# Optimization experiments

Hardware: AMD Instinct MI355X
Metric: run time of the kernel (lower is better)

The kernel has to match this reference:

```python
import jax, jax.numpy as jnp
import numpy as np

B = 512     # graphs
NPG = 128   # nodes per graph
EPG = 2048  # edges per graph (avg degree 16)
IN = 128
HID = 128
K = 64      # ceil(0.5 * 128), SAGPooling ratio=0.5


def setup_inputs() -> dict:
    key = jax.random.key(0)
    ks = jax.random.split(key, 8)
    n_total = B * NPG
    x = jax.random.normal(ks[0], (n_total, IN), dtype=jnp.float32)
    # intra-graph random edges (PyG batching: edges never cross graphs)
    g = jnp.repeat(jnp.arange(B, dtype=jnp.int32), EPG)
    src = g * NPG + jax.random.randint(ks[1], (B * EPG,), 0, NPG, dtype=jnp.int32)
    dst = g * NPG + jax.random.randint(ks[2], (B * EPG,), 0, NPG, dtype=jnp.int32)
    edge_index = jnp.stack([src, dst], axis=0)
    batch = jnp.repeat(jnp.arange(B, dtype=jnp.int32), NPG)
    # params (glorot-ish scaling)
    W1 = jax.random.normal(ks[3], (IN, HID), dtype=jnp.float32) / np.sqrt(IN)
    b1 = jnp.zeros((HID,), dtype=jnp.float32)
    Ws = jax.random.normal(ks[4], (HID, 1), dtype=jnp.float32) / np.sqrt(HID)
    bs = jnp.zeros((1,), dtype=jnp.float32)
    Wlin = jax.random.normal(ks[5], (HID, HID), dtype=jnp.float32) / np.sqrt(HID)
    blin = jnp.zeros((HID,), dtype=jnp.float32)
    return {"x": x, "edge_index": edge_index, "batch": batch,
            "W1": W1, "b1": b1, "Ws": Ws, "bs": bs, "Wlin": Wlin, "blin": blin}


def _gcn_conv(x, src, dst, W, b, n):
    # PyG GCNConv: add self loops, symmetric deg^-1/2 norm, aggregate src->dst
    h = x @ W  # [n, out]
    loop = jnp.arange(n, dtype=src.dtype)
    s = jnp.concatenate([src, loop])
    d = jnp.concatenate([dst, loop])
    deg = jax.ops.segment_sum(jnp.ones(d.shape[0], dtype=x.dtype), d, num_segments=n)
    norm = jax.lax.rsqrt(deg)[s] * jax.lax.rsqrt(deg)[d]  # deg >= 1 via self loops
    msg = h[s] * norm[:, None]
    return jax.ops.segment_sum(msg, d, num_segments=n) + b


def reference(x, edge_index, batch, W1, b1, Ws, bs, Wlin, blin):
    n = x.shape[0]
    src, dst = edge_index[0], edge_index[1]
    # conv1 + relu
    h = jax.nn.relu(_gcn_conv(x, src, dst, W1, b1, n))  # [n, HID]
    # SAGPooling: score via GCNConv(HID -> 1)
    score = _gcn_conv(h, src, dst, Ws, bs, n)[:, 0]  # [n]
    # per-graph top-k on raw score (graphs are uniform NPG nodes -> dense top_k)
    score2 = score.reshape(B, NPG)
    top_v, top_i = jax.lax.top_k(score2, K)  # [B, K]
    h3 = h.reshape(B, NPG, HID)
    h_kept = jnp.take_along_axis(h3, top_i[:, :, None], axis=1)  # [B, K, HID]
    h_kept = h_kept * jnp.tanh(top_v)[:, :, None]  # x[perm] * tanh(score[perm])
    # global_mean_pool over kept nodes of each graph
    pooled = h_kept.mean(axis=1)  # [B, HID]
    return pooled @ Wlin + blin
```

## Files before the change

kernel.cpp:

```cpp
#include <hip/hip_runtime.h>
#include <math.h>

#define NPG  128
#define HID  128
#define KSEL 64
#define NT   256
#define HS   132
#define AS   17
#define FS   516

typedef __attribute__((ext_vector_type(8))) __bf16 bfrag;
typedef __attribute__((ext_vector_type(4))) float f4;

static __device__ __forceinline__ unsigned short bf2us(__bf16 b) {
    union { unsigned short s; __bf16 b; } x; x.b = b; return x.s;
}

__global__ __launch_bounds__(NT, 2) void sagpool_fused(
    const float* __restrict__ x,
    const int*   __restrict__ esrc,
    const int*   __restrict__ edst,
    const float* __restrict__ W1,
    const float* __restrict__ b1,
    const float* __restrict__ Ws,
    const float* __restrict__ bsp,
    const float* __restrict__ Wlin,
    const float* __restrict__ blin,
    float* __restrict__ out,
    int epg)
{
    __shared__ __align__(16) unsigned HpT[HID * HS];
    __shared__ __align__(16) unsigned AdjN[NPG * AS];
    __shared__ __align__(16) float rsl[NPG];
    __shared__ __align__(16) float spl[NPG];
    __shared__ __align__(16) float scl[NPG];
    __shared__ __align__(16) float wgt[NPG];
    __shared__ __align__(16) float pp[4 * HID];

    const int g = blockIdx.x, t = threadIdx.x;
    const int node0 = g * NPG;
    const long e0 = (long)g * epg;
    const int lane = t & 63, wv = t >> 6;
    const int n16 = lane & 15, quad = lane >> 4;
    const int m0 = wv * 32;

    int es[8], ed[8];
#pragma unroll
    for (int i = 0; i < 8; ++i) {
        int e = i * NT + t;
        es[i] = esrc[e0 + e] - node0;
        ed[i] = edst[e0 + e] - node0;
    }
    bfrag ah[8], al[8];
    {
        const float* xw = x + (long)(node0 + m0) * HID;
#pragma unroll
        for (int rt = 0; rt < 2; ++rt)
#pragma unroll
            for (int ks = 0; ks < 4; ++ks) {
                const float* xr = xw + (rt * 16 + n16) * HID + ks * 32 + quad * 8;
                float4 a = *reinterpret_cast<const float4*>(xr);
                float4 b = *reinterpret_cast<const float4*>(xr + 4);
                float vv[8] = {a.x, a.y, a.z, a.w, b.x, b.y, b.z, b.w};
                const int r = rt * 4 + ks;
#pragma unroll
                for (int j = 0; j < 8; ++j) {
                    __bf16 hb = (__bf16)vv[j];
                    ah[r][j] = hb;
                    al[r][j] = (__bf16)(vv[j] - (float)hb);
                }
            }
    }
    float b1v[8], wsv[8];
#pragma unroll
    for (int ct = 0; ct < 8; ++ct) {
        b1v[ct] = b1[ct * 16 + n16];
        wsv[ct] = Ws[ct * 16 + n16];
    }
    const float bsv = bsp[0];

    for (int i = t; i < NPG * AS; i += NT) AdjN[i] = 0u;
    __syncthreads();

    {
#pragma unroll
        for (int i = 0; i < 4; ++i) {
            const int tau = i * NT + t;
            const int ng = tau & 31, kg = tau >> 5;
            const int n0 = ng * 4, k0 = kg * 4;
            f4 r[4];
#pragma unroll
            for (int e = 0; e < 4; ++e)
                r[e] = *reinterpret_cast<const f4*>(W1 + (k0 + e) * HID + n0);
            const int p   = (k0 >> 5) * 8 + (n0 >> 4);
            const int j0h = (k0 & 7) >> 1;
            const int l0  = ((k0 >> 3) & 3) * 16;
#pragma unroll
            for (int c = 0; c < 4; ++c) {
                const int lane0 = l0 + (n0 & 15) + c;
                unsigned hs[4], ls[4];
#pragma unroll
                for (int e = 0; e < 4; ++e) {
                    float v = r[e][c];
                    __bf16 hb = (__bf16)v;
                    __bf16 lb = (__bf16)(v - (float)hb);
                    hs[e] = bf2us(hb); ls[e] = bf2us(lb);
                }
                uint2 sh, sl;
                sh.x = hs[0] | (hs[1] << 16); sh.y = hs[2] | (hs[3] << 16);
                sl.x = ls[0] | (ls[1] << 16); sl.y = ls[2] | (ls[3] << 16);
                const int base = p * FS + lane0 * 4 + j0h;
                *reinterpret_cast<uint2*>(&HpT[base])       = sh;
                *reinterpret_cast<uint2*>(&HpT[base + 256]) = sl;
            }
        }
    }
#pragma unroll
    for (int i = 0; i < 8; ++i)
        atomicAdd(&AdjN[ed[i] * AS + (es[i] >> 3)], 1u << ((es[i] & 7) * 4));
    __syncthreads();

    if (t < NPG) {
        unsigned* row = &AdjN[t * AS];
        unsigned sum = 0;
#pragma unroll
        for (int w = 0; w < 16; ++w) {
            unsigned u = row[w];
            unsigned b = (u & 0x0F0F0F0Fu) + ((u >> 4) & 0x0F0F0F0Fu);
            sum += (b * 0x01010101u) >> 24;
        }
        rsl[t] = rsqrtf((float)(sum + 1));
        row[t >> 3] += 1u << ((t & 7) * 4);
    }

    f4 acc[2][8];
#pragma unroll
    for (int rt = 0; rt < 2; ++rt)
#pragma unroll
        for (int ct = 0; ct < 8; ++ct) {
            acc[rt][ct].x = 0.f; acc[rt][ct].y = 0.f;
            acc[rt][ct].z = 0.f; acc[rt][ct].w = 0.f;
        }
#pragma unroll
    for (int ks = 0; ks < 4; ++ks)
#pragma unroll
        for (int ct = 0; ct < 8; ++ct) {
            const unsigned* fp = &HpT[(ks * 8 + ct) * FS + lane * 4];
            bfrag bh = *reinterpret_cast<const bfrag*>(fp);
            bfrag bl = *reinterpret_cast<const bfrag*>(fp + 256);
#pragma unroll
            for (int rt = 0; rt < 2; ++rt) {
                const int r = rt * 4 + ks;
                acc[rt][ct] = __builtin_amdgcn_mfma_f32_16x16x32_bf16(ah[r], bh, acc[rt][ct], 0, 0, 0);
                acc[rt][ct] = __builtin_amdgcn_mfma_f32_16x16x32_bf16(al[r], bh, acc[rt][ct], 0, 0, 0);
                acc[rt][ct] = __builtin_amdgcn_mfma_f32_16x16x32_bf16(ah[r], bl, acc[rt][ct], 0, 0, 0);
            }
        }
    __syncthreads();

#pragma unroll
    for (int rt = 0; rt < 2; ++rt) {
        const int mb = m0 + rt * 16 + quad * 4;
        f4 rs4 = *reinterpret_cast<const f4*>(&rsl[mb]);
#pragma unroll
        for (int ct = 0; ct < 8; ++ct) {
            unsigned hs[4], ls[4];
#pragma unroll
            for (int reg = 0; reg < 4; ++reg) {
                float v = acc[rt][ct][reg] * rs4[reg];
                __bf16 hb = (__bf16)v;
                __bf16 lb = (__bf16)(v - (float)hb);
                hs[reg] = bf2us(hb); ls[reg] = bf2us(lb);
            }
            uint2 sh, sl;
            sh.x = hs[0] | (hs[1] << 16); sh.y = hs[2] | (hs[3] << 16);
            sl.x = ls[0] | (ls[1] << 16); sl.y = ls[2] | (ls[3] << 16);
            const int rb = (ct * 16 + n16) * HS + (mb >> 1);
            *reinterpret_cast<uint2*>(&HpT[rb])      = sh;
            *reinterpret_cast<uint2*>(&HpT[rb + 64]) = sl;
        }
    }
    __syncthreads();

    f4 hacc[2][8];
#pragma unroll
    for (int mt = 0; mt < 2; ++mt)
#pragma unroll
        for (int ct = 0; ct < 8; ++ct) {
            hacc[mt][ct].x = 0.f; hacc[mt][ct].y = 0.f;
            hacc[mt][ct].z = 0.f; hacc[mt][ct].w = 0.f;
        }
#pragma unroll
    for (int ks = 0; ks < 4; ++ks) {
        bfrag af[2];
#pragma unroll
        for (int mt = 0; mt < 2; ++mt) {
            unsigned w = AdjN[(m0 + mt * 16 + n16) * AS + ks * 4 + quad];
#pragma unroll
            for (int j = 0; j < 8; ++j)
                af[mt][j] = (__bf16)(float)((w >> (4 * j)) & 15u);
        }
#pragma unroll
        for (int ct = 0; ct < 8; ++ct) {
            const unsigned* bp = &HpT[(ct * 16 + n16) * HS + ks * 16 + quad * 4];
            bfrag bh = *reinterpret_cast<const bfrag*>(bp);
            bfrag bl = *reinterpret_cast<const bfrag*>(bp + 64);
#pragma unroll
            for (int mt = 0; mt < 2; ++mt) {
                hacc[mt][ct] = __builtin_amdgcn_mfma_f32_16x16x32_bf16(af[mt], bh, hacc[mt][ct], 0, 0, 0);
                hacc[mt][ct] = __builtin_amdgcn_mfma_f32_16x16x32_bf16(af[mt], bl, hacc[mt][ct], 0, 0, 0);
            }
        }
    }

    f4 rsm[2];
#pragma unroll
    for (int mt = 0; mt < 2; ++mt)
        rsm[mt] = *reinterpret_cast<const f4*>(&rsl[m0 + mt * 16 + quad * 4]);
#pragma unroll
    for (int mt = 0; mt < 2; ++mt)
#pragma unroll
        for (int ct = 0; ct < 8; ++ct)
#pragma unroll
            for (int reg = 0; reg < 4; ++reg)
                hacc[mt][ct][reg] = fmaxf(hacc[mt][ct][reg] * rsm[mt][reg] + b1v[ct], 0.f);

    {
        float dot[2][4];
#pragma unroll
        for (int mt = 0; mt < 2; ++mt)
#pragma unroll
            for (int reg = 0; reg < 4; ++reg) dot[mt][reg] = 0.f;
#pragma unroll
        for (int ct = 0; ct < 8; ++ct)
#pragma unroll
            for (int mt = 0; mt < 2; ++mt)
#pragma unroll
                for (int reg = 0; reg < 4; ++reg)
                    dot[mt][reg] += hacc[mt][ct][reg] * wsv[ct];
#pragma unroll
        for (int d = 1; d < 16; d <<= 1)
#pragma unroll
            for (int mt = 0; mt < 2; ++mt)
#pragma unroll
                for (int reg = 0; reg < 4; ++reg)
                    dot[mt][reg] += __shfl_xor(dot[mt][reg], d, 64);
        if (n16 == 0) {
#pragma unroll
            for (int mt = 0; mt < 2; ++mt)
#pragma unroll
                for (int reg = 0; reg < 4; ++reg)
                    spl[m0 + mt * 16 + quad * 4 + reg] = rsm[mt][reg] * dot[mt][reg];
        }
    }
    __syncthreads();

    if (t < NPG) {
        const unsigned* row = &AdjN[t * AS];
        float sc = 0.f;
#pragma unroll
        for (int w = 0; w < 16; ++w) {
            unsigned u = row[w];
            const float* sp = &spl[w * 8];
            sc += (float)(u & 15u)         * sp[0] + (float)((u >> 4)  & 15u) * sp[1]
                + (float)((u >> 8)  & 15u) * sp[2] + (float)((u >> 12) & 15u) * sp[3]
                + (float)((u >> 16) & 15u) * sp[4] + (float)((u >> 20) & 15u) * sp[5]
                + (float)((u >> 24) & 15u) * sp[6] + (float)(u >> 28)         * sp[7];
        }
        scl[t] = rsl[t] * sc + bsv;
    } else {
        const int tt = t - NPG;
        const f4* WL4 = reinterpret_cast<const f4*>(Wlin);
        for (int ib = 0; ib < 4; ++ib) {
            f4 w[8];
#pragma unroll
            for (int u = 0; u < 8; ++u)
                w[u] = WL4[(ib * 8 + u) * 128 + tt];
#pragma unroll
            for (int u = 0; u < 8; ++u)
                *reinterpret_cast<f4*>(&HpT[((ib * 8 + u) * 128 + tt) * 4]) = w[u];
        }
    }
    __syncthreads();

    if (t < NPG) {
        float v = scl[t];
        int rank = 0;
#pragma unroll
        for (int j4 = 0; j4 < 32; ++j4) {
            float4 u = *reinterpret_cast<const float4*>(&scl[j4 * 4]);
            const int jb = j4 * 4;
            rank += (u.x > v || (u.x == v && jb     < t)) ? 1 : 0;
            rank += (u.y > v || (u.y == v && jb + 1 < t)) ? 1 : 0;
            rank += (u.z > v || (u.z == v && jb + 2 < t)) ? 1 : 0;
            rank += (u.w > v || (u.w == v && jb + 3 < t)) ? 1 : 0;
        }
        wgt[t] = (rank < KSEL) ? tanhf(v) * (1.0f / KSEL) : 0.f;
    }
    __syncthreads();

    {
        float p[8];
        f4 wm[2];
#pragma unroll
        for (int mt = 0; mt < 2; ++mt)
            wm[mt] = *reinterpret_cast<const f4*>(&wgt[m0 + mt * 16 + quad * 4]);
#pragma unroll
        for (int ct = 0; ct < 8; ++ct) {
            float s = 0.f;
#pragma unroll
            for (int mt = 0; mt < 2; ++mt)
#pragma unroll
                for (int reg = 0; reg < 4; ++reg)
                    s += wm[mt][reg] * hacc[mt][ct][reg];
            p[ct] = s;
        }
#pragma unroll
        for (int d = 16; d < 64; d <<= 1)
#pragma unroll
            for (int ct = 0; ct < 8; ++ct)
                p[ct] += __shfl_xor(p[ct], d, 64);
        if (quad == 0) {
#pragma unroll
            for (int ct = 0; ct < 8; ++ct)
                pp[wv * HID + ct * 16 + n16] = p[ct];
        }
    }
    __syncthreads();
    if (t < NPG)
        scl[t] = pp[t] + pp[HID + t] + pp[2 * HID + t] + pp[3 * HID + t];
    __syncthreads();

    {
        const int c4 = (t & 31) * 4, rg = t >> 5;
        f4 s4; s4.x = 0.f; s4.y = 0.f; s4.z = 0.f; s4.w = 0.f;
#pragma unroll 8
        for (int kk = 0; kk < 16; ++kk) {
            const int k = rg * 16 + kk;
            const f4 w = *reinterpret_cast<const f4*>(&HpT[k * HID + c4]);
            const float sk = scl[k];
            s4.x += sk * w.x; s4.y += sk * w.y;
            s4.z += sk * w.z; s4.w += sk * w.w;
        }
        float* part = reinterpret_cast<float*>(AdjN);
        *reinterpret_cast<f4*>(&part[rg * HID + c4]) = s4;
    }
    __syncthreads();
    if (t < NPG) {
        const float* part = reinterpret_cast<const float*>(AdjN);
        float s = blin[t];
#pragma unroll
        for (int r = 0; r < 8; ++r) s += part[r * HID + t];
        out[(long)g * HID + t] = s;
    }
}

extern "C" void kernel_launch(void* const* d_in, const int* in_sizes, int n_in,
                              void* d_out, int out_size, void* d_ws, size_t ws_size,
                              hipStream_t stream) {
    const float* x    = (const float*)d_in[0];
    const int*   ei   = (const int*)  d_in[1];
    const float* W1   = (const float*)d_in[3];
    const float* b1   = (const float*)d_in[4];
    const float* Ws   = (const float*)d_in[5];
    const float* bs   = (const float*)d_in[6];
    const float* Wlin = (const float*)d_in[7];
    const float* blin = (const float*)d_in[8];
    float* out = (float*)d_out;

    const int E = in_sizes[1] / 2;
    const int nnodes = in_sizes[0] / HID;
    const int B = nnodes / NPG;
    const int epg = E / B;

    sagpool_fused<<<B, NT, 0, stream>>>(x, ei, ei + E, W1, b1, Ws, bs,
                                        Wlin, blin, out, epg);
}
```

Measured before the change: 108.3 us.

## Double block size and split output column tiles across two wave groups

Raises the block to 512 threads (8 waves) and has each pair of waves split the 128 output columns in half. Both dense MFMA stages (x@W1 and the adjacency aggregation) and the pooling reduction now use half the column tiles per wave, with score partials summed from two shared-memory slices. Edge loading, W1 staging and the final Wlin product are redistributed across the extra threads. The aim is more waves per CU to hide latency, at the cost of each column half reloading the same x rows and a tighter register budget under launch_bounds(512,4), which may cause spills.

Measured after the change: 113.6 us. +4.9%, slower.

```diff
diff --git a/kernel.cpp b/kernel.cpp
--- a/kernel.cpp
+++ b/kernel.cpp
@@ -4,7 +4,7 @@
 #define NPG  128
 #define HID  128
 #define KSEL 64
-#define NT   256
+#define NT   512
 #define HS   132
 #define AS   17
 #define FS   516
@@ -16,7 +16,7 @@
     union { unsigned short s; __bf16 b; } x; x.b = b; return x.s;
 }
 
-__global__ __launch_bounds__(NT, 2) void sagpool_fused(
+__global__ __launch_bounds__(NT, 4) void sagpool_fused(
     const float* __restrict__ x,
     const int*   __restrict__ esrc,
     const int*   __restrict__ edst,
@@ -32,7 +32,7 @@
     __shared__ __align__(16) unsigned HpT[HID * HS];
     __shared__ __align__(16) unsigned AdjN[NPG * AS];
     __shared__ __align__(16) float rsl[NPG];
-    __shared__ __align__(16) float spl[NPG];
+    __shared__ __align__(16) float spl[2 * NPG];
     __shared__ __align__(16) float scl[NPG];
     __shared__ __align__(16) float wgt[NPG];
     __shared__ __align__(16) float pp[4 * HID];
@@ -41,12 +41,13 @@
     const int node0 = g * NPG;
     const long e0 = (long)g * epg;
     const int lane = t & 63, wv = t >> 6;
+    const int rt4 = wv & 3, ch = wv >> 2;
     const int n16 = lane & 15, quad = lane >> 4;
-    const int m0 = wv * 32;
-
-    int es[8], ed[8];
-#pragma unroll
-    for (int i = 0; i < 8; ++i) {
+    const int m0 = rt4 * 32;
+
+    int es[4], ed[4];
+#pragma unroll
+    for (int i = 0; i < 4; ++i) {
         int e = i * NT + t;
         es[i] = esrc[e0 + e] - node0;
         ed[i] = edst[e0 + e] - node0;
@@ -71,20 +72,13 @@
                 }
             }
     }
-    float b1v[8], wsv[8];
-#pragma unroll
-    for (int ct = 0; ct < 8; ++ct) {
-        b1v[ct] = b1[ct * 16 + n16];
-        wsv[ct] = Ws[ct * 16 + n16];
-    }
-    const float bsv = bsp[0];
 
     for (int i = t; i < NPG * AS; i += NT) AdjN[i] = 0u;
     __syncthreads();
 
     {
 #pragma unroll
-        for (int i = 0; i < 4; ++i) {
+        for (int i = 0; i < 2; ++i) {
             const int tau = i * NT + t;
             const int ng = tau & 31, kg = tau >> 5;
             const int n0 = ng * 4, k0 = kg * 4;
@@ -116,7 +110,7 @@
         }
     }
 #pragma unroll
-    for (int i = 0; i < 8; ++i)
+    for (int i = 0; i < 4; ++i)
         atomicAdd(&AdjN[ed[i] * AS + (es[i] >> 3)], 1u << ((es[i] & 7) * 4));
     __syncthreads();
 
@@ -133,27 +127,28 @@
         row[t >> 3] += 1u << ((t & 7) * 4);
     }
 
-    f4 acc[2][8];
+    f4 acc[2][4];
 #pragma unroll
     for (int rt = 0; rt < 2; ++rt)
 #pragma unroll
-        for (int ct = 0; ct < 8; ++ct) {
-            acc[rt][ct].x = 0.f; acc[rt][ct].y = 0.f;
-            acc[rt][ct].z = 0.f; acc[rt][ct].w = 0.f;
+        for (int c = 0; c < 4; ++c) {
+            acc[rt][c].x = 0.f; acc[rt][c].y = 0.f;
+            acc[rt][c].z = 0.f; acc[rt][c].w = 0.f;
         }
 #pragma unroll
     for (int ks = 0; ks < 4; ++ks)
 #pragma unroll
-        for (int ct = 0; ct < 8; ++ct) {
-            const unsigned* fp = &HpT[(ks * 8 + ct) * FS + lane * 4];
+        for (int c = 0; c < 4; ++c) {
+            const int ctg = ch * 4 + c;
+            const unsigned* fp = &HpT[(ks * 8 + ctg) * FS + lane * 4];
             bfrag bh = *reinterpret_cast<const bfrag*>(fp);
             bfrag bl = *reinterpret_cast<const bfrag*>(fp + 256);
 #pragma unroll
             for (int rt = 0; rt < 2; ++rt) {
                 const int r = rt * 4 + ks;
-                acc[rt][ct] = __builtin_amdgcn_mfma_f32_16x16x32_bf16(ah[r], bh, acc[rt][ct], 0, 0, 0);
-                acc[rt][ct] = __builtin_amdgcn_mfma_f32_16x16x32_bf16(al[r], bh, acc[rt][ct], 0, 0, 0);
-                acc[rt][ct] = __builtin_amdgcn_mfma_f32_16x16x32_bf16(ah[r], bl, acc[rt][ct], 0, 0, 0);
+                acc[rt][c] = __builtin_amdgcn_mfma_f32_16x16x32_bf16(ah[r], bh, acc[rt][c], 0, 0, 0);
+                acc[rt][c] = __builtin_amdgcn_mfma_f32_16x16x32_bf16(al[r], bh, acc[rt][c], 0, 0, 0);
+                acc[rt][c] = __builtin_amdgcn_mfma_f32_16x16x32_bf16(ah[r], bl, acc[rt][c], 0, 0, 0);
             }
         }
     __syncthreads();
@@ -163,11 +158,12 @@
         const int mb = m0 + rt * 16 + quad * 4;
         f4 rs4 = *reinterpret_cast<const f4*>(&rsl[mb]);
 #pragma unroll
-        for (int ct = 0; ct < 8; ++ct) {
+        for (int c = 0; c < 4; ++c) {
+            const int ctg = ch * 4 + c;
             unsigned hs[4], ls[4];
 #pragma unroll
             for (int reg = 0; reg < 4; ++reg) {
-                float v = acc[rt][ct][reg] * rs4[reg];
+                float v = acc[rt][c][reg] * rs4[reg];
                 __bf16 hb = (__bf16)v;
                 __bf16 lb = (__bf16)(v - (float)hb);
                 hs[reg] = bf2us(hb); ls[reg] = bf2us(lb);
@@ -175,110 +171,121 @@
             uint2 sh, sl;
             sh.x = hs[0] | (hs[1] << 16); sh.y = hs[2] | (hs[3] << 16);
             sl.x = ls[0] | (ls[1] << 16); sl.y = ls[2] | (ls[3] << 16);
-            const int rb = (ct * 16 + n16) * HS + (mb >> 1);
+            const int rb = (ctg * 16 + n16) * HS + (mb >> 1);
             *reinterpret_cast<uint2*>(&HpT[rb])      = sh;
             *reinterpret_cast<uint2*>(&HpT[rb + 64]) = sl;
         }
     }
     __syncthreads();
 
-    f4 hacc[2][8];
-#pragma unroll
-    for (int mt = 0; mt < 2; ++mt)
-#pragma unroll
-        for (int ct = 0; ct < 8; ++ct) {
-            hacc[mt][ct].x = 0.f; hacc[mt][ct].y = 0.f;
-            hacc[mt][ct].z = 0.f; hacc[mt][ct].w = 0.f;
+    float b1v[4], wsv[4];
+#pragma unroll
+    for (int c = 0; c < 4; ++c) {
+        b1v[c] = b1[(ch * 4 + c) * 16 + n16];
+        wsv[c] = Ws[(ch * 4 + c) * 16 + n16];
+    }
+    const float bsv = bsp[0];
+
+    f4 hacc[2][4];
+#pragma unroll
+    for (int rt = 0; rt < 2; ++rt)
+#pragma unroll
+        for (int c = 0; c < 4; ++c) {
+            hacc[rt][c].x = 0.f; hacc[rt][c].y = 0.f;
+            hacc[rt][c].z = 0.f; hacc[rt][c].w = 0.f;
         }
 #pragma unroll
     for (int ks = 0; ks < 4; ++ks) {
         bfrag af[2];
 #pragma unroll
-        for (int mt = 0; mt < 2; ++mt) {
-            unsigned w = AdjN[(m0 + mt * 16 + n16) * AS + ks * 4 + quad];
+        for (int rt = 0; rt < 2; ++rt) {
+            unsigned w = AdjN[(m0 + rt * 16 + n16) * AS + ks * 4 + quad];
 #pragma unroll
             for (int j = 0; j < 8; ++j)
-                af[mt][j] = (__bf16)(float)((w >> (4 * j)) & 15u);
-        }
-#pragma unroll
-        for (int ct = 0; ct < 8; ++ct) {
-            const unsigned* bp = &HpT[(ct * 16 + n16) * HS + ks * 16 + quad * 4];
+                af[rt][j] = (__bf16)(float)((w >> (4 * j)) & 15u);
+        }
+#pragma unroll
+        for (int c = 0; c < 4; ++c) {
+            const int ctg = ch * 4 + c;
+            const unsigned* bp = &HpT[(ctg * 16 + n16) * HS + ks * 16 + quad * 4];
             bfrag bh = *reinterpret_cast<const bfrag*>(bp);
             bfrag bl = *reinterpret_cast<const bfrag*>(bp + 64);
 #pragma unroll
-            for (int mt = 0; mt < 2; ++mt) {
-                hacc[mt][ct] = __builtin_amdgcn_mfma_f32_16x16x32_bf16(af[mt], bh, hacc[mt][ct], 0, 0, 0);
-                hacc[mt][ct] = __builtin_amdgcn_mfma_f32_16x16x32_bf16(af[mt], bl, hacc[mt][ct], 0, 0, 0);
+            for (int rt = 0; rt < 2; ++rt) {
+                hacc[rt][c] = __builtin_amdgcn_mfma_f32_16x16x32_bf16(af[rt], bh, hacc[rt][c], 0, 0, 0);
+                hacc[rt][c] = __builtin_amdgcn_mfma_f32_16x16x32_bf16(af[rt], bl, hacc[rt][c], 0, 0, 0);
             }
         }
     }
 
     f4 rsm[2];
 #pragma unroll
-    for (int mt = 0; mt < 2; ++mt)
-        rsm[mt] = *reinterpret_cast<const f4*>(&rsl[m0 + mt * 16 + quad * 4]);
-#pragma unroll
-    for (int mt = 0; mt < 2; ++mt)
-#pragma unroll
-        for (int ct = 0; ct < 8; ++ct)
+    for (int rt = 0; rt < 2; ++rt)
+        rsm[rt] = *reinterpret_cast<const f4*>(&rsl[m0 + rt * 16 + quad * 4]);
+#pragma unroll
+    for (int rt = 0; rt < 2; ++rt)
+#pragma unroll
+        for (int c = 0; c < 4; ++c)
 #pragma unroll
             for (int reg = 0; reg < 4; ++reg)
-                hacc[mt][ct][reg] = fmaxf(hacc[mt][ct][reg] * rsm[mt][reg] + b1v[ct], 0.f);
+                hacc[rt][c][reg] = fmaxf(hacc[rt][c][reg] * rsm[rt][reg] + b1v[c], 0.f);
 
     {
         float dot[2][4];
 #pragma unroll
-        for (int mt = 0; mt < 2; ++mt)
-#pragma unroll
-            for (int reg = 0; reg < 4; ++reg) dot[mt][reg] = 0.f;
-#pragma unroll
-        for (int ct = 0; ct < 8; ++ct)
-#pragma unroll
-            for (int mt = 0; mt < 2; ++mt)
+        for (int rt = 0; rt < 2; ++rt)
+#pragma unroll
+            for (int reg = 0; reg < 4; ++reg) dot[rt][reg] = 0.f;
+#pragma unroll
+        for (int c = 0; c < 4; ++c)
+#pragma unroll
+            for (int rt = 0; rt < 2; ++rt)
 #pragma unroll
                 for (int reg = 0; reg < 4; ++reg)
-                    dot[mt][reg] += hacc[mt][ct][reg] * wsv[ct];
+                    dot[rt][reg] += hacc[rt][c][reg] * wsv[c];
 #pragma unroll
         for (int d = 1; d < 16; d <<= 1)
 #pragma unroll
-            for (int mt = 0; mt < 2; ++mt)
+            for (int rt = 0; rt < 2; ++rt)
 #pragma unroll
                 for (int reg = 0; reg < 4; ++reg)
-                    dot[mt][reg] += __shfl_xor(dot[mt][reg], d, 64);
+                    dot[rt][reg] += __shfl_xor(dot[rt][reg], d, 64);
         if (n16 == 0) {
 #pragma unroll
-            for (int mt = 0; mt < 2; ++mt)
+            for (int rt = 0; rt < 2; ++rt)
 #pragma unroll
                 for (int reg = 0; reg < 4; ++reg)
-                    spl[m0 + mt * 16 + quad * 4 + reg] = rsm[mt][reg] * dot[mt][reg];
+                    spl[ch * NPG + m0 + rt * 16 + quad * 4 + reg] = rsm[rt][reg] * dot[rt][reg];
         }
     }
     __syncthreads();
 
     if (t < NPG) {
         const unsigned* row = &AdjN[t * AS];
+        const float* sp0 = spl;
+        const float* sp1 = spl + NPG;
         float sc = 0.f;
 #pragma unroll
         for (int w = 0; w < 16; ++w) {
             unsigned u = row[w];
-            const float* sp = &spl[w * 8];
-            sc += (float)(u & 15u)         * sp[0] + (float)((u >> 4)  & 15u) * sp[1]
-                + (float)((u >> 8)  & 15u) * sp[2] + (float)((u >> 12) & 15u) * sp[3]
-                + (float)((u >> 16) & 15u) * sp[4] + (float)((u >> 20) & 15u) * sp[5]
-                + (float)((u >> 24) & 15u) * sp[6] + (float)(u >> 28)         * sp[7];
+            const int b8 = w * 8;
+            sc += (float)(u & 15u)         * (sp0[b8]     + sp1[b8])
+                + (float)((u >> 4)  & 15u) * (sp0[b8 + 1] + sp1[b8 + 1])
+                + (float)((u >> 8)  & 15u) * (sp0[b8 + 2] + sp1[b8 + 2])
+                + (float)((u >> 12) & 15u) * (sp0[b8 + 3] + sp1[b8 + 3])
+                + (float)((u >> 16) & 15u) * (sp0[b8 + 4] + sp1[b8 + 4])
+                + (float)((u >> 20) & 15u) * (sp0[b8 + 5] + sp1[b8 + 5])
+                + (float)((u >> 24) & 15u) * (sp0[b8 + 6] + sp1[b8 + 6])
+                + (float)(u >> 28)         * (sp0[b8 + 7] + sp1[b8 + 7]);
         }
         scl[t] = rsl[t] * sc + bsv;
-    } else {
-        const int tt = t - NPG;
+    } else if (t < 384) {
+        const int ts = t - NPG;
         const f4* WL4 = reinterpret_cast<const f4*>(Wlin);
-        for (int ib = 0; ib < 4; ++ib) {
-            f4 w[8];
-#pragma unroll
-            for (int u = 0; u < 8; ++u)
-                w[u] = WL4[(ib * 8 + u) * 128 + tt];
-#pragma unroll
-            for (int u = 0; u < 8; ++u)
-                *reinterpret_cast<f4*>(&HpT[((ib * 8 + u) * 128 + tt) * 4]) = w[u];
+#pragma unroll
+        for (int i = 0; i < 16; ++i) {
+            const int fd = i * 256 + ts;
+            *reinterpret_cast<f4*>(&HpT[fd * 4]) = WL4[fd];
         }
     }
     __syncthreads();
@@ -300,30 +307,30 @@
     __syncthreads();
 
     {
-        float p[8];
+        float p[4];
         f4 wm[2];
 #pragma unroll
-        for (int mt = 0; mt < 2; ++mt)
-            wm[mt] = *reinterpret_cast<const f4*>(&wgt[m0 + mt * 16 + quad * 4]);
-#pragma unroll
-        for (int ct = 0; ct < 8; ++ct) {
+        for (int rt = 0; rt < 2; ++rt)
+            wm[rt] = *reinterpret_cast<const f4*>(&wgt[m0 + rt * 16 + quad * 4]);
+#pragma unroll
+        for (int c = 0; c < 4; ++c) {
             float s = 0.f;
 #pragma unroll
-            for (int mt = 0; mt < 2; ++mt)
+            for (int rt = 0; rt < 2; ++rt)
 #pragma unroll
                 for (int reg = 0; reg < 4; ++reg)
-                    s += wm[mt][reg] * hacc[mt][ct][reg];
-            p[ct] = s;
+                    s += wm[rt][reg] * hacc[rt][c][reg];
+            p[c] = s;
         }
 #pragma unroll
         for (int d = 16; d < 64; d <<= 1)
 #pragma unroll
-            for (int ct = 0; ct < 8; ++ct)
-                p[ct] += __shfl_xor(p[ct], d, 64);
+            for (int c = 0; c < 4; ++c)
+                p[c] += __shfl_xor(p[c], d, 64);
         if (quad == 0) {
 #pragma unroll
-            for (int ct = 0; ct < 8; ++ct)
-                pp[wv * HID + ct * 16 + n16] = p[ct];
+            for (int c = 0; c < 4; ++c)
+                pp[rt4 * HID + (ch * 4 + c) * 16 + n16] = p[c];
         }
     }
     __syncthreads();
@@ -334,9 +341,9 @@
     {
         const int c4 = (t & 31) * 4, rg = t >> 5;
         f4 s4; s4.x = 0.f; s4.y = 0.f; s4.z = 0.f; s4.w = 0.f;
-#pragma unroll 8
-        for (int kk = 0; kk < 16; ++kk) {
-            const int k = rg * 16 + kk;
+#pragma unroll
+        for (int kk = 0; kk < 8; ++kk) {
+            const int k = rg * 8 + kk;
             const f4 w = *reinterpret_cast<const f4*>(&HpT[k * HID + c4]);
             const float sk = scl[k];
             s4.x += sk * w.x; s4.y += sk * w.y;
@@ -350,7 +357,7 @@
         const float* part = reinterpret_cast<const float*>(AdjN);
         float s = blin[t];
 #pragma unroll
-        for (int r = 0; r < 8; ++r) s += part[r * HID + t];
+        for (int r = 0; r < 16; ++r) s += part[r * HID + t];
         out[(long)g * HID + t] = s;
     }
 }
```

## Cut block barriers by computing norms and top-k ranks per wave with lane shuffles

Applied to the files above, without the earlier changes.

Each wave now computes the degree norms and top-k ranks for its own 32 rows, splitting the work across both wave halves and combining with shuffles. Results are broadcast to the MFMA lane layout with ds_bpermute, which removes the shared-memory round trips and several __syncthreads. The two GEMM phases are chunked over column pairs, so bf16 packing and the ReLU/score dot product are fused into the MFMA loops. A fast exp-based tanh replaces tanhf, and the final partial-sum reduction is folded into the Wlin matvec to drop another barrier. The cost is extra registers for the packed outputs and precomputed adjacency fragments, which may hurt occupancy, and the tanh approximation is slightly less accurate.

New measurement: 108.7 us. Within noise of the previous version (+0.4%).

```diff
diff --git a/kernel.cpp b/kernel.cpp
--- a/kernel.cpp
+++ b/kernel.cpp
@@ -14,6 +14,10 @@
 
 static __device__ __forceinline__ unsigned short bf2us(__bf16 b) {
     union { unsigned short s; __bf16 b; } x; x.b = b; return x.s;
+}
+static __device__ __forceinline__ float fast_tanh(float v) {
+    float e = __expf(2.f * v);
+    return 1.f - 2.f * __builtin_amdgcn_rcpf(e + 1.f);
 }
 
 __global__ __launch_bounds__(NT, 2) void sagpool_fused(
@@ -34,7 +38,6 @@
     __shared__ __align__(16) float rsl[NPG];
     __shared__ __align__(16) float spl[NPG];
     __shared__ __align__(16) float scl[NPG];
-    __shared__ __align__(16) float wgt[NPG];
     __shared__ __align__(16) float pp[4 * HID];
 
     const int g = blockIdx.x, t = threadIdx.x;
@@ -42,6 +45,7 @@
     const long e0 = (long)g * epg;
     const int lane = t & 63, wv = t >> 6;
     const int n16 = lane & 15, quad = lane >> 4;
+    const int l2 = lane & 31, half = lane >> 5;
     const int m0 = wv * 32;
 
     int es[8], ed[8];
@@ -120,124 +124,144 @@
         atomicAdd(&AdjN[ed[i] * AS + (es[i] >> 3)], 1u << ((es[i] & 7) * 4));
     __syncthreads();
 
-    if (t < NPG) {
-        unsigned* row = &AdjN[t * AS];
+    f4 rs4[2];
+    {
+        const unsigned* row = &AdjN[(m0 + l2) * AS + half * 8];
         unsigned sum = 0;
 #pragma unroll
-        for (int w = 0; w < 16; ++w) {
+        for (int w = 0; w < 8; ++w) {
             unsigned u = row[w];
             unsigned b = (u & 0x0F0F0F0Fu) + ((u >> 4) & 0x0F0F0F0Fu);
             sum += (b * 0x01010101u) >> 24;
         }
-        rsl[t] = rsqrtf((float)(sum + 1));
-        row[t >> 3] += 1u << ((t & 7) * 4);
-    }
-
-    f4 acc[2][8];
-#pragma unroll
-    for (int rt = 0; rt < 2; ++rt)
-#pragma unroll
-        for (int ct = 0; ct < 8; ++ct) {
-            acc[rt][ct].x = 0.f; acc[rt][ct].y = 0.f;
-            acc[rt][ct].z = 0.f; acc[rt][ct].w = 0.f;
-        }
+        sum += (unsigned)__shfl_xor((int)sum, 32, 64);
+        float rs = rsqrtf((float)(sum + 1));
+        if (lane < 32) rsl[m0 + lane] = rs;
+        const int rvi = __float_as_int(rs);
+#pragma unroll
+        for (int rt = 0; rt < 2; ++rt)
+#pragma unroll
+            for (int reg = 0; reg < 4; ++reg)
+                rs4[rt][reg] = __int_as_float(
+                    __builtin_amdgcn_ds_bpermute(4 * (rt * 16 + quad * 4 + reg), rvi));
+    }
+
+    uint2 shp[2][8], slp[2][8];
+#pragma unroll
+    for (int ctp = 0; ctp < 4; ++ctp) {
+        f4 a2[2][2];
+#pragma unroll
+        for (int rt = 0; rt < 2; ++rt)
+#pragma unroll
+            for (int cc = 0; cc < 2; ++cc) {
+                a2[rt][cc].x = 0.f; a2[rt][cc].y = 0.f;
+                a2[rt][cc].z = 0.f; a2[rt][cc].w = 0.f;
+            }
+#pragma unroll
+        for (int ks = 0; ks < 4; ++ks)
+#pragma unroll
+            for (int cc = 0; cc < 2; ++cc) {
+                const int ct = ctp * 2 + cc;
+                const unsigned* fp = &HpT[(ks * 8 + ct) * FS + lane * 4];
+                bfrag bh = *reinterpret_cast<const bfrag*>(fp);
+                bfrag bl = *reinterpret_cast<const bfrag*>(fp + 256);
+#pragma unroll
+                for (int rt = 0; rt < 2; ++rt) {
+                    const int r = rt * 4 + ks;
+                    a2[rt][cc] = __builtin_amdgcn_mfma_f32_16x16x32_bf16(ah[r], bh, a2[rt][cc], 0, 0, 0);
+                    a2[rt][cc] = __builtin_amdgcn_mfma_f32_16x16x32_bf16(al[r], bh, a2[rt][cc], 0, 0, 0);
+                    a2[rt][cc] = __builtin_amdgcn_mfma_f32_16x16x32_bf16(ah[r], bl, a2[rt][cc], 0, 0, 0);
+                }
+            }
+#pragma unroll
+        for (int rt = 0; rt < 2; ++rt)
+#pragma unroll
+            for (int cc = 0; cc < 2; ++cc) {
+                const int ct = ctp * 2 + cc;
+                unsigned hs[4], ls[4];
+#pragma unroll
+                for (int reg = 0; reg < 4; ++reg) {
+                    float v = a2[rt][cc][reg] * rs4[rt][reg];
+                    __bf16 hb = (__bf16)v;
+                    __bf16 lb = (__bf16)(v - (float)hb);
+                    hs[reg] = bf2us(hb); ls[reg] = bf2us(lb);
+                }
+                shp[rt][ct].x = hs[0] | (hs[1] << 16); shp[rt][ct].y = hs[2] | (hs[3] << 16);
+                slp[rt][ct].x = ls[0] | (ls[1] << 16); slp[rt][ct].y = ls[2] | (ls[3] << 16);
+            }
+    }
+    __syncthreads();
+
+    {
+        const int mbh = (m0 >> 1) + quad * 2;
+#pragma unroll
+        for (int rt = 0; rt < 2; ++rt)
+#pragma unroll
+            for (int ct = 0; ct < 8; ++ct) {
+                const int rb = (ct * 16 + n16) * HS + mbh + rt * 8;
+                *reinterpret_cast<uint2*>(&HpT[rb])      = shp[rt][ct];
+                *reinterpret_cast<uint2*>(&HpT[rb + 64]) = slp[rt][ct];
+            }
+    }
+    if (t < NPG)
+        AdjN[t * AS + (t >> 3)] += 1u << ((t & 7) * 4);
+    __syncthreads();
+
+    bfrag af[4][2];
 #pragma unroll
     for (int ks = 0; ks < 4; ++ks)
-#pragma unroll
-        for (int ct = 0; ct < 8; ++ct) {
-            const unsigned* fp = &HpT[(ks * 8 + ct) * FS + lane * 4];
-            bfrag bh = *reinterpret_cast<const bfrag*>(fp);
-            bfrag bl = *reinterpret_cast<const bfrag*>(fp + 256);
-#pragma unroll
-            for (int rt = 0; rt < 2; ++rt) {
-                const int r = rt * 4 + ks;
-                acc[rt][ct] = __builtin_amdgcn_mfma_f32_16x16x32_bf16(ah[r], bh, acc[rt][ct], 0, 0, 0);
-                acc[rt][ct] = __builtin_amdgcn_mfma_f32_16x16x32_bf16(al[r], bh, acc[rt][ct], 0, 0, 0);
-                acc[rt][ct] = __builtin_amdgcn_mfma_f32_16x16x32_bf16(ah[r], bl, acc[rt][ct], 0, 0, 0);
-            }
-        }
-    __syncthreads();
-
-#pragma unroll
-    for (int rt = 0; rt < 2; ++rt) {
-        const int mb = m0 + rt * 16 + quad * 4;
-        f4 rs4 = *reinterpret_cast<const f4*>(&rsl[mb]);
-#pragma unroll
-        for (int ct = 0; ct < 8; ++ct) {
-            unsigned hs[4], ls[4];
-#pragma unroll
-            for (int reg = 0; reg < 4; ++reg) {
-                float v = acc[rt][ct][reg] * rs4[reg];
-                __bf16 hb = (__bf16)v;
-                __bf16 lb = (__bf16)(v - (float)hb);
-                hs[reg] = bf2us(hb); ls[reg] = bf2us(lb);
-            }
-            uint2 sh, sl;
-            sh.x = hs[0] | (hs[1] << 16); sh.y = hs[2] | (hs[3] << 16);
-            sl.x = ls[0] | (ls[1] << 16); sl.y = ls[2] | (ls[3] << 16);
-            const int rb = (ct * 16 + n16) * HS + (mb >> 1);
-            *reinterpret_cast<uint2*>(&HpT[rb])      = sh;
-            *reinterpret_cast<uint2*>(&HpT[rb + 64]) = sl;
-        }
-    }
-    __syncthreads();
-
-    f4 hacc[2][8];
-#pragma unroll
-    for (int mt = 0; mt < 2; ++mt)
-#pragma unroll
-        for (int ct = 0; ct < 8; ++ct) {
-            hacc[mt][ct].x = 0.f; hacc[mt][ct].y = 0.f;
-            hacc[mt][ct].z = 0.f; hacc[mt][ct].w = 0.f;
-        }
-#pragma unroll
-    for (int ks = 0; ks < 4; ++ks) {
-        bfrag af[2];
 #pragma unroll
         for (int mt = 0; mt < 2; ++mt) {
             unsigned w = AdjN[(m0 + mt * 16 + n16) * AS + ks * 4 + quad];
 #pragma unroll
             for (int j = 0; j < 8; ++j)
-                af[mt][j] = (__bf16)(float)((w >> (4 * j)) & 15u);
-        }
-#pragma unroll
-        for (int ct = 0; ct < 8; ++ct) {
-            const unsigned* bp = &HpT[(ct * 16 + n16) * HS + ks * 16 + quad * 4];
-            bfrag bh = *reinterpret_cast<const bfrag*>(bp);
-            bfrag bl = *reinterpret_cast<const bfrag*>(bp + 64);
-#pragma unroll
-            for (int mt = 0; mt < 2; ++mt) {
-                hacc[mt][ct] = __builtin_amdgcn_mfma_f32_16x16x32_bf16(af[mt], bh, hacc[mt][ct], 0, 0, 0);
-                hacc[mt][ct] = __builtin_amdgcn_mfma_f32_16x16x32_bf16(af[mt], bl, hacc[mt][ct], 0, 0, 0);
-            }
-        }
-    }
-
-    f4 rsm[2];
+                af[ks][mt][j] = (__bf16)(float)((w >> (4 * j)) & 15u);
+        }
+    f4 hacc[2][8];
+    float dot[2][4];
 #pragma unroll
     for (int mt = 0; mt < 2; ++mt)
-        rsm[mt] = *reinterpret_cast<const f4*>(&rsl[m0 + mt * 16 + quad * 4]);
-#pragma unroll
-    for (int mt = 0; mt < 2; ++mt)
-#pragma unroll
-        for (int ct = 0; ct < 8; ++ct)
-#pragma unroll
-            for (int reg = 0; reg < 4; ++reg)
-                hacc[mt][ct][reg] = fmaxf(hacc[mt][ct][reg] * rsm[mt][reg] + b1v[ct], 0.f);
-
-    {
-        float dot[2][4];
+#pragma unroll
+        for (int reg = 0; reg < 4; ++reg) dot[mt][reg] = 0.f;
+#pragma unroll
+    for (int ctp = 0; ctp < 4; ++ctp) {
 #pragma unroll
         for (int mt = 0; mt < 2; ++mt)
 #pragma unroll
-            for (int reg = 0; reg < 4; ++reg) dot[mt][reg] = 0.f;
-#pragma unroll
-        for (int ct = 0; ct < 8; ++ct)
-#pragma unroll
-            for (int mt = 0; mt < 2; ++mt)
-#pragma unroll
-                for (int reg = 0; reg < 4; ++reg)
-                    dot[mt][reg] += hacc[mt][ct][reg] * wsv[ct];
+            for (int cc = 0; cc < 2; ++cc) {
+                const int ct = ctp * 2 + cc;
+                hacc[mt][ct].x = 0.f; hacc[mt][ct].y = 0.f;
+                hacc[mt][ct].z = 0.f; hacc[mt][ct].w = 0.f;
+            }
+#pragma unroll
+        for (int ks = 0; ks < 4; ++ks)
+#pragma unroll
+            for (int cc = 0; cc < 2; ++cc) {
+                const int ct = ctp * 2 + cc;
+                const unsigned* bp = &HpT[(ct * 16 + n16) * HS + ks * 16 + quad * 4];
+                bfrag bh = *reinterpret_cast<const bfrag*>(bp);
+                bfrag bl = *reinterpret_cast<const bfrag*>(bp + 64);
+#pragma unroll
+                for (int mt = 0; mt < 2; ++mt) {
+                    hacc[mt][ct] = __builtin_amdgcn_mfma_f32_16x16x32_bf16(af[ks][mt], bh, hacc[mt][ct], 0, 0, 0);
+                    hacc[mt][ct] = __builtin_amdgcn_mfma_f32_16x16x32_bf16(af[ks][mt], bl, hacc[mt][ct], 0, 0, 0);
+                }
+            }
+#pragma unroll
+        for (int mt = 0; mt < 2; ++mt)
+#pragma unroll
+            for (int cc = 0; cc < 2; ++cc) {
+                const int ct = ctp * 2 + cc;
+#pragma unroll
+                for (int reg = 0; reg < 4; ++reg) {
+                    float v = fmaxf(hacc[mt][ct][reg] * rs4[mt][reg] + b1v[ct], 0.f);
+                    hacc[mt][ct][reg] = v;
+                    dot[mt][reg] += v * wsv[ct];
+                }
+            }
+    }
+
+    {
 #pragma unroll
         for (int d = 1; d < 16; d <<= 1)
 #pragma unroll
@@ -250,7 +274,7 @@
             for (int mt = 0; mt < 2; ++mt)
 #pragma unroll
                 for (int reg = 0; reg < 4; ++reg)
-                    spl[m0 + mt * 16 + quad * 4 + reg] = rsm[mt][reg] * dot[mt][reg];
+                    spl[m0 + mt * 16 + quad * 4 + reg] = rs4[mt][reg] * dot[mt][reg];
         }
     }
     __syncthreads();
@@ -271,40 +295,46 @@
     } else {
         const int tt = t - NPG;
         const f4* WL4 = reinterpret_cast<const f4*>(Wlin);
-        for (int ib = 0; ib < 4; ++ib) {
-            f4 w[8];
-#pragma unroll
-            for (int u = 0; u < 8; ++u)
-                w[u] = WL4[(ib * 8 + u) * 128 + tt];
-#pragma unroll
-            for (int u = 0; u < 8; ++u)
-                *reinterpret_cast<f4*>(&HpT[((ib * 8 + u) * 128 + tt) * 4]) = w[u];
-        }
-    }
-    __syncthreads();
-
-    if (t < NPG) {
-        float v = scl[t];
+#pragma unroll
+        for (int b2 = 0; b2 < 2; ++b2) {
+            f4 w[16];
+#pragma unroll
+            for (int u = 0; u < 16; ++u)
+                w[u] = WL4[(b2 * 16 + u) * 128 + tt];
+#pragma unroll
+            for (int u = 0; u < 16; ++u)
+                *reinterpret_cast<f4*>(&HpT[((b2 * 16 + u) * 128 + tt) * 4]) = w[u];
+        }
+    }
+    __syncthreads();
+
+    float wm[2][4];
+    {
+        const int nd = m0 + l2;
+        float v = scl[nd];
         int rank = 0;
 #pragma unroll
-        for (int j4 = 0; j4 < 32; ++j4) {
-            float4 u = *reinterpret_cast<const float4*>(&scl[j4 * 4]);
-            const int jb = j4 * 4;
-            rank += (u.x > v || (u.x == v && jb     < t)) ? 1 : 0;
-            rank += (u.y > v || (u.y == v && jb + 1 < t)) ? 1 : 0;
-            rank += (u.z > v || (u.z == v && jb + 2 < t)) ? 1 : 0;
-            rank += (u.w > v || (u.w == v && jb + 3 < t)) ? 1 : 0;
-        }
-        wgt[t] = (rank < KSEL) ? tanhf(v) * (1.0f / KSEL) : 0.f;
-    }
-    __syncthreads();
+        for (int j4 = 0; j4 < 16; ++j4) {
+            const int jb = half * 64 + j4 * 4;
+            float4 u = *reinterpret_cast<const float4*>(&scl[jb]);
+            rank += (u.x > v || (u.x == v && jb     < nd)) ? 1 : 0;
+            rank += (u.y > v || (u.y == v && jb + 1 < nd)) ? 1 : 0;
+            rank += (u.z > v || (u.z == v && jb + 2 < nd)) ? 1 : 0;
+            rank += (u.w > v || (u.w == v && jb + 3 < nd)) ? 1 : 0;
+        }
+        rank += __shfl_xor(rank, 32, 64);
+        float wfull = (rank < KSEL) ? fast_tanh(v) * (1.0f / KSEL) : 0.f;
+        const int wvi = __float_as_int(wfull);
+#pragma unroll
+        for (int mt = 0; mt < 2; ++mt)
+#pragma unroll
+            for (int reg = 0; reg < 4; ++reg)
+                wm[mt][reg] = __int_as_float(
+                    __builtin_amdgcn_ds_bpermute(4 * (mt * 16 + quad * 4 + reg), wvi));
+    }
 
     {
         float p[8];
-        f4 wm[2];
-#pragma unroll
-        for (int mt = 0; mt < 2; ++mt)
-            wm[mt] = *reinterpret_cast<const f4*>(&wgt[m0 + mt * 16 + quad * 4]);
 #pragma unroll
         for (int ct = 0; ct < 8; ++ct) {
             float s = 0.f;
@@ -326,9 +356,6 @@
                 pp[wv * HID + ct * 16 + n16] = p[ct];
         }
     }
-    __syncthreads();
-    if (t < NPG)
-        scl[t] = pp[t] + pp[HID + t] + pp[2 * HID + t] + pp[3 * HID + t];
     __syncthreads();
 
     {
@@ -337,8 +364,8 @@
 #pragma unroll 8
         for (int kk = 0; kk < 16; ++kk) {
             const int k = rg * 16 + kk;
+            const float sk = pp[k] + pp[HID + k] + pp[2 * HID + k] + pp[3 * HID + k];
             const f4 w = *reinterpret_cast<const f4*>(&HpT[k * HID + c4]);
-            const float sk = scl[k];
             s4.x += sk * w.x; s4.y += sk * w.y;
             s4.z += sk * w.z; s4.w += sk * w.w;
         }
```
